# Optimization experiments

Measured on AMD Instinct MI355X. Metric: run time of the kernel, lower is better.

The kernel has to match this reference:

```python
import jax, jax.numpy as jnp
import numpy as np

V = 32000; D = 1024; H = 16; L = 2; T = 2048; B = 4; C = 32000
DH = D // H
EPS = 1e-5


def layernorm(x, g, b):
    mu = jnp.mean(x, axis=-1, keepdims=True)
    var = jnp.mean((x - mu) ** 2, axis=-1, keepdims=True)
    return (x - mu) * jax.lax.rsqrt(var + EPS) * g + b


def setup_inputs() -> dict:
    key = jax.random.key(0)
    ks = jax.random.split(key, 16)
    s = 0.02
    return {
        "tokens": jax.random.randint(ks[0], (B, T), 0, V),
        "embed_W": jax.random.normal(ks[1], (V, D), jnp.float32) * s,
        "pos_W": jax.random.normal(ks[2], (T, D), jnp.float32) * s,
        "ln_g": jnp.ones((L, D), jnp.float32),
        "ln_b": jnp.zeros((L, D), jnp.float32),
        "qkv_W": jax.random.normal(ks[3], (L, D, 3 * D), jnp.float32) * s,
        "qkv_b": jnp.zeros((L, 3 * D), jnp.float32),
        "out_W": jax.random.normal(ks[4], (L, D, D), jnp.float32) * s,
        "out_b": jnp.zeros((L, D), jnp.float32),
        "lnf_g": jnp.ones((D,), jnp.float32),
        "lnf_b": jnp.zeros((D,), jnp.float32),
        "head_W": jax.random.normal(ks[5], (D, C), jnp.float32) * s,
        "head_b": jnp.zeros((C,), jnp.float32),
    }


def attn_block(x, g, b, Wqkv, bqkv, Wo, bo):
    # pre-LN attention + residual. NOTE: original module defines an MLP but never calls it.
    h = layernorm(x, g, b)
    qkv = h @ Wqkv + bqkv                      # [B,T,3D]
    q, k, v = jnp.split(qkv, 3, axis=-1)
    q = q.reshape(B, T, H, DH)
    k = k.reshape(B, T, H, DH)
    v = v.reshape(B, T, H, DH)
    scores = jnp.einsum("bqhd,bkhd->bhqk", q, k) / np.sqrt(DH)
    causal = jnp.tril(jnp.ones((T, T), bool))
    scores = jnp.where(causal, scores, -jnp.inf)
    attn = jax.nn.softmax(scores, axis=-1)
    o = jnp.einsum("bhqk,bkhd->bqhd", attn, v).reshape(B, T, D)
    return x + o @ Wo + bo


def reference(tokens, embed_W, pos_W, ln_g, ln_b, qkv_W, qkv_b, out_W, out_b,
              lnf_g, lnf_b, head_W, head_b):
    h = embed_W[tokens] + pos_W[jnp.arange(T)][None, :, :]   # [B,T,D]
    for i in range(L):
        h = attn_block(h, ln_g[i], ln_b[i], qkv_W[i], qkv_b[i], out_W[i], out_b[i])
    h = layernorm(h, lnf_g, lnf_b)
    logits = h[:, -1] @ head_W + head_b                      # [B,C]
    return logits
```

## Files before the change

kernel.cpp:

```cpp
#include <hip/hip_runtime.h>

typedef __attribute__((ext_vector_type(8))) __bf16 bf16x8;
typedef __attribute__((ext_vector_type(4))) __bf16 bf16x4;
typedef __attribute__((ext_vector_type(4))) float f32x4;
typedef unsigned long long ull;

static constexpr int kB = 4, kT = 2048, kD = 1024, kH = 16;
static constexpr int kC = 32000, kM = 8192, k3D = 3072, kQK = 2048;

#define MFMA16(a, b, c) __builtin_amdgcn_mfma_f32_16x16x32_bf16((a), (b), (c), 0, 0, 0)

__device__ __forceinline__ void gload_lds16(const __bf16* g, __bf16* l) {
  __builtin_amdgcn_global_load_lds(
      (const __attribute__((address_space(1))) unsigned int*)(const void*)g,
      (__attribute__((address_space(3))) unsigned int*)(void*)l, 16, 0, 0);
}

__global__ __launch_bounds__(256) void prep_kernel(const float* __restrict__ qkv_W,
                                                   const float* __restrict__ out_W,
                                                   __bf16* __restrict__ WqkvT,
                                                   __bf16* __restrict__ WoT,
                                                   const int* __restrict__ tok,
                                                   const float* __restrict__ embW,
                                                   const float* __restrict__ posW,
                                                   const float* __restrict__ g,
                                                   const float* __restrict__ bb,
                                                   float* __restrict__ h,
                                                   __bf16* __restrict__ hn) {
  const int bid = blockIdx.x, tid = threadIdx.x;
  if (bid < 7168) {
    __shared__ float sh[32][33];
    const float* W; __bf16* WT; int N, tile;
    if (bid < 3072)      { W = qkv_W;                  WT = WqkvT;                  N = k3D; tile = bid; }
    else if (bid < 6144) { W = qkv_W + (size_t)kD*k3D; WT = WqkvT + (size_t)k3D*kD; N = k3D; tile = bid - 3072; }
    else                 { W = out_W;                  WT = WoT;                    N = kD;  tile = bid - 6144; }
    const int tx = tid & 31, ty = tid >> 5;
    const int ntile = N >> 5;
    const int c0 = (tile % ntile) << 5;
    const int r0 = (tile / ntile) << 5;
    #pragma unroll
    for (int i = 0; i < 4; i++) {
      const int r = ty + i * 8;
      sh[r][tx] = W[(size_t)(r0 + r) * N + c0 + tx];
    }
    __syncthreads();
    #pragma unroll
    for (int i = 0; i < 4; i++) {
      const int cc = ty + i * 8;
      WT[(size_t)(c0 + cc) * kD + r0 + tx] = (__bf16)sh[tx][cc];
    }
  } else {
    const int row = bid - 7168;
    const int t = row & (kT - 1);
    const int tk = tok[row];
    const f32x4 e = ((const f32x4*)(embW + (size_t)tk * kD))[tid];
    const f32x4 p = ((const f32x4*)(posW + (size_t)t * kD))[tid];
    const f32x4 xv = e + p;
    ((f32x4*)(h + (size_t)row * kD))[tid] = xv;
    float s  = xv[0] + xv[1] + xv[2] + xv[3];
    float s2 = xv[0]*xv[0] + xv[1]*xv[1] + xv[2]*xv[2] + xv[3]*xv[3];
    #pragma unroll
    for (int off = 1; off < 64; off <<= 1) {
      s  += __shfl_xor(s, off);
      s2 += __shfl_xor(s2, off);
    }
    __shared__ float red[8];
    const int w = tid >> 6;
    if ((tid & 63) == 0) { red[w*2] = s; red[w*2+1] = s2; }
    __syncthreads();
    s  = red[0] + red[2] + red[4] + red[6];
    s2 = red[1] + red[3] + red[5] + red[7];
    const float mu  = s * (1.f / kD);
    const float var = s2 * (1.f / kD) - mu * mu;
    const float rs  = rsqrtf(var + 1e-5f);
    const f32x4 gv = ((const f32x4*)g)[tid];
    const f32x4 bv = ((const f32x4*)bb)[tid];
    bf16x4 o;
    #pragma unroll
    for (int i = 0; i < 4; i++) o[i] = (__bf16)((xv[i] - mu) * rs * gv[i] + bv[i]);
    ((bf16x4*)(hn + (size_t)row * kD))[tid] = o;
  }
}

template <bool BF16OUT>
__global__ __launch_bounds__(256) void ln_kernel(const float* __restrict__ x,
                                                 const float* __restrict__ g,
                                                 const float* __restrict__ bb,
                                                 void* __restrict__ outp) {
  const int row = blockIdx.x, tid = threadIdx.x;
  const f32x4 xv = ((const f32x4*)(x + (size_t)row * kD))[tid];
  float s  = xv[0] + xv[1] + xv[2] + xv[3];
  float s2 = xv[0]*xv[0] + xv[1]*xv[1] + xv[2]*xv[2] + xv[3]*xv[3];
  #pragma unroll
  for (int off = 1; off < 64; off <<= 1) {
    s  += __shfl_xor(s, off);
    s2 += __shfl_xor(s2, off);
  }
  __shared__ float red[8];
  const int w = tid >> 6;
  if ((tid & 63) == 0) { red[w*2] = s; red[w*2+1] = s2; }
  __syncthreads();
  s  = red[0] + red[2] + red[4] + red[6];
  s2 = red[1] + red[3] + red[5] + red[7];
  const float mu  = s * (1.f / kD);
  const float var = s2 * (1.f / kD) - mu * mu;
  const float rs  = rsqrtf(var + 1e-5f);
  const f32x4 gv = ((const f32x4*)g)[tid];
  const f32x4 bv = ((const f32x4*)bb)[tid];
  if constexpr (BF16OUT) {
    bf16x4 o;
    #pragma unroll
    for (int i = 0; i < 4; i++) o[i] = (__bf16)((xv[i] - mu) * rs * gv[i] + bv[i]);
    ((bf16x4*)((__bf16*)outp + (size_t)row * kD))[tid] = o;
  } else {
    f32x4 o;
    #pragma unroll
    for (int i = 0; i < 4; i++) o[i] = (xv[i] - mu) * rs * gv[i] + bv[i];
    ((f32x4*)((float*)outp + (size_t)row * kD))[tid] = o;
  }
}

template <bool OUT_BF16>
__global__ __launch_bounds__(256) void gemm_bt_kernel(const __bf16* __restrict__ A,
                                                      const __bf16* __restrict__ BT,
                                                      const float* __restrict__ bias,
                                                      const float* resid,
                                                      float* outf,
                                                      __bf16* outb,
                                                      __bf16* vtp,
                                                      int N, int K, int ldc, int vt_c0,
                                                      int bm_mult, int bm_add) {
  __shared__ __bf16 As[128 * 64];
  __shared__ __bf16 Bs[128 * 64];
  const int tid = threadIdx.x;
  const int lane = tid & 63, w = tid >> 6;
  int wg = (int)blockIdx.x;
  const int nwg = gridDim.x;
  wg = (wg & 7) * (nwg >> 3) + (wg >> 3);
  const int nbn = N >> 7;
  const int bm = (wg / nbn) * bm_mult + bm_add;
  const int bn = wg % nbn;
  const int wr = (w >> 1) * 64, wc = (w & 1) * 64;
  const int lrow = lane & 15, lk8 = (lane >> 4) * 8;

  const int srow = lane >> 3;
  const int scol = (lane & 7) * 8;
  const __bf16* gA = A + (size_t)(bm * 128) * K;
  const __bf16* gB = BT + (size_t)(bn * 128) * K;

  f32x4 acc[4][4] = {};

  for (int k0 = 0; k0 < K; k0 += 64) {
    __syncthreads();
    #pragma unroll
    for (int i = 0; i < 4; i++) {
      const int c = w * 4 + i;
      const int row = c * 8 + srow;
      gload_lds16(gA + (size_t)row * K + k0 + scol, As + c * 512);
      gload_lds16(gB + (size_t)row * K + k0 + scol, Bs + c * 512);
    }
    __syncthreads();
    #pragma unroll
    for (int ks = 0; ks < 2; ks++) {
      bf16x8 af[4], bf[4];
      #pragma unroll
      for (int mt = 0; mt < 4; mt++)
        af[mt] = *(const bf16x8*)(As + (wr + mt * 16 + lrow) * 64 + ks * 32 + lk8);
      #pragma unroll
      for (int nt = 0; nt < 4; nt++)
        bf[nt] = *(const bf16x8*)(Bs + (wc + nt * 16 + lrow) * 64 + ks * 32 + lk8);
      __builtin_amdgcn_s_setprio(1);
      #pragma unroll
      for (int mt = 0; mt < 4; mt++)
        #pragma unroll
        for (int nt = 0; nt < 4; nt++)
          acc[mt][nt] = MFMA16(af[mt], bf[nt], acc[mt][nt]);
      __builtin_amdgcn_s_setprio(0);
    }
  }

  #pragma unroll
  for (int mt = 0; mt < 4; mt++) {
    const int row0 = bm * 128 + wr + mt * 16 + (lane >> 4) * 4;
    #pragma unroll
    for (int nt = 0; nt < 4; nt++) {
      const int col = bn * 128 + wc + nt * 16 + lrow;
      const float bsv = bias[col];
      if (vtp && col >= vt_c0) {
        const int vd = col - vt_c0;
        const int bb_ = row0 >> 11, t = row0 & (kT - 1);
        bf16x4 pk;
        #pragma unroll
        for (int r = 0; r < 4; r++) pk[r] = (__bf16)(acc[mt][nt][r] + bsv);
        *(bf16x4*)(vtp + ((size_t)((bb_ << 4) + (vd >> 6)) * 64 + (vd & 63)) * kT + t) = pk;
      } else {
        #pragma unroll
        for (int r = 0; r < 4; r++) {
          const size_t idx = (size_t)(row0 + r) * ldc + col;
          const float v = acc[mt][nt][r] + bsv;
          if constexpr (OUT_BF16) {
            outb[idx] = (__bf16)v;
          } else {
            outf[idx] = v + resid[idx];
          }
        }
      }
    }
  }
}

__global__ __launch_bounds__(256) void flash0_kernel(const __bf16* __restrict__ qkv,
                                                     const __bf16* __restrict__ vtg,
                                                     __bf16* __restrict__ o) {
  constexpr float SC = 0.18033688011112042f;
  __shared__ __bf16 Ks[64 * 64];
  __shared__ __bf16 Vs[64 * 64];
  const int tid = threadIdx.x, lane = tid & 63, w = tid >> 6;
  int wg = (int)blockIdx.x;
  const int nwg = gridDim.x;
  wg = (wg & 7) * (nwg >> 3) + (wg >> 3);
  const int sub = wg & 15, bh = wg >> 4;
  const int b = bh >> 4, hh = bh & 15;
  const int g = lane >> 4, qown = lane & 15;
  const int r8 = lane >> 3;
  const int sslot = (lane & 7) ^ (r8 & 7);
  const int swz = (qown & 7) << 3;
  const size_t row0 = (size_t)b * kT;

  for (int s = 0; s < 2; s++) {
    const int qt = s ? (31 - sub) : sub;

    const __bf16* qrow = qkv + (row0 + qt * 64 + w * 16 + qown) * kQK + hh * 64;
    bf16x8 qf[2];
    #pragma unroll
    for (int ks = 0; ks < 2; ks++) {
      bf16x8 qr = *(const bf16x8*)(qrow + ks * 32 + 8 * g);
      #pragma unroll
      for (int i = 0; i < 8; i++) qf[ks][i] = (__bf16)((float)qr[i] * SC);
    }

    float m_run = -1e30f, l_run = 0.f;
    f32x4 acc[4] = {};

    for (int kt = 0; kt <= qt; kt++) {
      __syncthreads();
      #pragma unroll
      for (int j = 0; j < 2; j++) {
        const int r = w * 16 + j * 8 + r8;
        gload_lds16(qkv + (row0 + kt * 64 + r) * kQK + 1024 + hh * 64 + sslot * 8,
                    Ks + (w * 16 + j * 8) * 64);
        gload_lds16(vtg + ((size_t)bh * 64 + r) * kT + kt * 64 + sslot * 8,
                    Vs + (w * 16 + j * 8) * 64);
      }
      __syncthreads();

      f32x4 sv[4] = {};
      #pragma unroll
      for (int nt = 0; nt < 4; nt++) {
        const int kr = nt * 16 + qown;
        #pragma unroll
        for (int ks = 0; ks < 2; ks++) {
          bf16x8 kf = *(const bf16x8*)(Ks + kr * 64 + ((ks * 32 + 8 * g) ^ swz));
          sv[nt] = MFMA16(kf, qf[ks], sv[nt]);
        }
      }
      if (kt == qt) {
        #pragma unroll
        for (int nt = 0; nt < 4; nt++)
          #pragma unroll
          for (int r = 0; r < 4; r++)
            if (nt * 16 + 4 * g + r > w * 16 + qown) sv[nt][r] = -1e30f;
      }

      float mx = -1e30f;
      #pragma unroll
      for (int nt = 0; nt < 4; nt++)
        #pragma unroll
        for (int r = 0; r < 4; r++) mx = fmaxf(mx, sv[nt][r]);
      mx = fmaxf(mx, __shfl_xor(mx, 16));
      mx = fmaxf(mx, __shfl_xor(mx, 32));

      float ps = 0.f;
      ull quad[4];
      if (__all(mx - m_run <= 8.0f)) {
        #pragma unroll
        for (int nt = 0; nt < 4; nt++) {
          union { bf16x4 v; ull u; } qd;
          #pragma unroll
          for (int r = 0; r < 4; r++) {
            const float p = exp2f(sv[nt][r] - m_run);
            ps += p;
            qd.v[r] = (__bf16)p;
          }
          quad[nt] = qd.u;
        }
        ps += __shfl_xor(ps, 16);
        ps += __shfl_xor(ps, 32);
        l_run += ps;
      } else {
        const float mnew = fmaxf(m_run, mx);
        const float fsc = exp2f(m_run - mnew);
        m_run = mnew;
        #pragma unroll
        for (int nt = 0; nt < 4; nt++) {
          union { bf16x4 v; ull u; } qd;
          #pragma unroll
          for (int r = 0; r < 4; r++) {
            const float p = exp2f(sv[nt][r] - mnew);
            ps += p;
            qd.v[r] = (__bf16)p;
          }
          quad[nt] = qd.u;
        }
        ps += __shfl_xor(ps, 16);
        ps += __shfl_xor(ps, 32);
        l_run = l_run * fsc + ps;
        float fr[4];
        #pragma unroll
        for (int r = 0; r < 4; r++) fr[r] = __shfl(fsc, 20 * g + r);
        #pragma unroll
        for (int nt = 0; nt < 4; nt++)
          #pragma unroll
          for (int r = 0; r < 4; r++) acc[nt][r] *= fr[r];
      }

      bf16x8 pf[2];
      #pragma unroll
      for (int ks = 0; ks < 2; ks++) {
        const int src = (g & 1) * 32 + qown;
        const ull t0 = __shfl(quad[2 * ks],     src);
        const ull t1 = __shfl(quad[2 * ks + 1], src);
        const ull lo = (g & 2) ? t1 : t0;
        const ull t2 = __shfl(quad[2 * ks],     src + 16);
        const ull t3 = __shfl(quad[2 * ks + 1], src + 16);
        const ull hi = (g & 2) ? t3 : t2;
        union { ull u[2]; bf16x8 v; } pk;
        pk.u[0] = lo; pk.u[1] = hi;
        pf[ks] = pk.v;
      }

      #pragma unroll
      for (int nt = 0; nt < 4; nt++) {
        const int vr = nt * 16 + qown;
        #pragma unroll
        for (int ks = 0; ks < 2; ks++) {
          bf16x8 vf = *(const bf16x8*)(Vs + vr * 64 + ((ks * 32 + 8 * g) ^ swz));
          acc[nt] = MFMA16(pf[ks], vf, acc[nt]);
        }
      }
    }

    const float li = 1.f / l_run;
    float lr[4];
    #pragma unroll
    for (int r = 0; r < 4; r++) lr[r] = __shfl(li, 20 * g + r);
    #pragma unroll
    for (int r = 0; r < 4; r++) {
      const int t = qt * 64 + w * 16 + 4 * g + r;
      #pragma unroll
      for (int nt = 0; nt < 4; nt++)
        o[(row0 + t) * kD + hh * 64 + nt * 16 + qown] = (__bf16)(acc[nt][r] * lr[r]);
    }
  }
}

__global__ __launch_bounds__(256) void flash1_kernel(const __bf16* __restrict__ qkv,
                                                     const __bf16* __restrict__ vtg,
                                                     float* __restrict__ part_acc,
                                                     float* __restrict__ part_ml) {
  constexpr float SC = 0.18033688011112042f;
  __shared__ __bf16 Ks[64 * 64];
  __shared__ __bf16 Vs[64 * 64];
  const int tid = threadIdx.x, lane = tid & 63, w = tid >> 6;
  int wg = (int)blockIdx.x;
  const int nwg = gridDim.x;
  wg = (wg & 7) * (nwg >> 3) + (wg >> 3);
  const int sub = wg & 7, bh = wg >> 3;
  const int b = bh >> 4, hh = bh & 15;
  const int g = lane >> 4, qown = lane & 15;
  const int r8 = lane >> 3;
  const int sslot = (lane & 7) ^ (r8 & 7);
  const int swz = (qown & 7) << 3;
  const size_t row0 = (size_t)b * kT;
  const int qt = 31, ktlo = sub * 4, kthi = ktlo + 4;

  const __bf16* qrow = qkv + (row0 + qt * 64 + w * 16 + qown) * kQK + hh * 64;
  bf16x8 qf[2];
  #pragma unroll
  for (int ks = 0; ks < 2; ks++) {
    bf16x8 qr = *(const bf16x8*)(qrow + ks * 32 + 8 * g);
    #pragma unroll
    for (int i = 0; i < 8; i++) qf[ks][i] = (__bf16)((float)qr[i] * SC);
  }

  float m_run = -1e30f, l_run = 0.f;
  f32x4 acc[4] = {};

  for (int kt = ktlo; kt < kthi; kt++) {
    __syncthreads();
    #pragma unroll
    for (int jj = 0; jj < 2; jj++) {
      const int r = w * 16 + jj * 8 + r8;
      gload_lds16(qkv + (row0 + kt * 64 + r) * kQK + 1024 + hh * 64 + sslot * 8,
                  Ks + (w * 16 + jj * 8) * 64);
      gload_lds16(vtg + ((size_t)bh * 64 + r) * kT + kt * 64 + sslot * 8,
                  Vs + (w * 16 + jj * 8) * 64);
    }
    __syncthreads();

    f32x4 sv[4] = {};
    #pragma unroll
    for (int nt = 0; nt < 4; nt++) {
      const int kr = nt * 16 + qown;
      #pragma unroll
      for (int ks = 0; ks < 2; ks++) {
        bf16x8 kf = *(const bf16x8*)(Ks + kr * 64 + ((ks * 32 + 8 * g) ^ swz));
        sv[nt] = MFMA16(kf, qf[ks], sv[nt]);
      }
    }
    if (kt == qt) {
      #pragma unroll
      for (int nt = 0; nt < 4; nt++)
        #pragma unroll
        for (int r = 0; r < 4; r++)
          if (nt * 16 + 4 * g + r > w * 16 + qown) sv[nt][r] = -1e30f;
    }

    float mx = -1e30f;
    #pragma unroll
    for (int nt = 0; nt < 4; nt++)
      #pragma unroll
      for (int r = 0; r < 4; r++) mx = fmaxf(mx, sv[nt][r]);
    mx = fmaxf(mx, __shfl_xor(mx, 16));
    mx = fmaxf(mx, __shfl_xor(mx, 32));

    const float mnew = fmaxf(m_run, mx);
    const float fsc = exp2f(m_run - mnew);
    m_run = mnew;
    float ps = 0.f;
    ull quad[4];
    #pragma unroll
    for (int nt = 0; nt < 4; nt++) {
      union { bf16x4 v; ull u; } qd;
      #pragma unroll
      for (int r = 0; r < 4; r++) {
        const float p = exp2f(sv[nt][r] - mnew);
        ps += p;
        qd.v[r] = (__bf16)p;
      }
      quad[nt] = qd.u;
    }
    ps += __shfl_xor(ps, 16);
    ps += __shfl_xor(ps, 32);
    l_run = l_run * fsc + ps;
    float fr[4];
    #pragma unroll
    for (int r = 0; r < 4; r++) fr[r] = __shfl(fsc, 20 * g + r);
    #pragma unroll
    for (int nt = 0; nt < 4; nt++)
      #pragma unroll
      for (int r = 0; r < 4; r++) acc[nt][r] *= fr[r];

    bf16x8 pf[2];
    #pragma unroll
    for (int ks = 0; ks < 2; ks++) {
      const int src = (g & 1) * 32 + qown;
      const ull t0 = __shfl(quad[2 * ks],     src);
      const ull t1 = __shfl(quad[2 * ks + 1], src);
      const ull lo = (g & 2) ? t1 : t0;
      const ull t2 = __shfl(quad[2 * ks],     src + 16);
      const ull t3 = __shfl(quad[2 * ks + 1], src + 16);
      const ull hi = (g & 2) ? t3 : t2;
      union { ull u[2]; bf16x8 v; } pk;
      pk.u[0] = lo; pk.u[1] = hi;
      pf[ks] = pk.v;
    }

    #pragma unroll
    for (int nt = 0; nt < 4; nt++) {
      const int vr = nt * 16 + qown;
      #pragma unroll
      for (int ks = 0; ks < 2; ks++) {
        bf16x8 vf = *(const bf16x8*)(Vs + vr * 64 + ((ks * 32 + 8 * g) ^ swz));
        acc[nt] = MFMA16(pf[ks], vf, acc[nt]);
      }
    }
  }

  const int tile = bh * 8 + sub;
  #pragma unroll
  for (int r = 0; r < 4; r++) {
    const int rr = w * 16 + 4 * g + r;
    #pragma unroll
    for (int nt = 0; nt < 4; nt++)
      part_acc[(size_t)tile * 4096 + rr * 64 + nt * 16 + qown] = acc[nt][r];
  }
  if (g == 0) {
    part_ml[tile * 128 + w * 16 + qown] = m_run;
    part_ml[tile * 128 + 64 + w * 16 + qown] = l_run;
  }
}

__global__ __launch_bounds__(256) void flash_merge_kernel(const float* __restrict__ part_acc,
                                                          const float* __restrict__ part_ml,
                                                          __bf16* __restrict__ o) {
  const int bh = blockIdx.x, b = bh >> 4, hh = bh & 15;
  for (int e = threadIdx.x; e < 4096; e += 256) {
    const int row = e >> 6, d = e & 63;
    float mstar = -1e30f;
    #pragma unroll
    for (int kc = 0; kc < 8; kc++)
      mstar = fmaxf(mstar, part_ml[(bh * 8 + kc) * 128 + row]);
    float lstar = 0.f, osum = 0.f;
    #pragma unroll
    for (int kc = 0; kc < 8; kc++) {
      const float wgt = exp2f(part_ml[(bh * 8 + kc) * 128 + row] - mstar);
      lstar += wgt * part_ml[(bh * 8 + kc) * 128 + 64 + row];
      osum  += wgt * part_acc[(size_t)(bh * 8 + kc) * 4096 + e];
    }
    o[(size_t)(b * kT + 1984 + row) * kD + hh * 64 + d] = (__bf16)(osum / lstar);
  }
}

__global__ __launch_bounds__(256) void proj_last_kernel(const __bf16* __restrict__ o,
                                                        const float* __restrict__ W,
                                                        const float* __restrict__ bias,
                                                        const float* __restrict__ h,
                                                        float* __restrict__ out4) {
  const int b = blockIdx.y;
  const int j = blockIdx.x * 256 + threadIdx.x;
  __shared__ float ov[kD];
  const __bf16* orow = o + (size_t)(b * kT + kT - 1) * kD;
  for (int i = threadIdx.x; i < kD; i += 256) ov[i] = (float)orow[i];
  __syncthreads();
  float acc = 0.f;
  #pragma unroll 8
  for (int k = 0; k < kD; k++) acc = fmaf(ov[k], W[(size_t)k * kD + j], acc);
  out4[b * kD + j] = h[(size_t)(b * kT + kT - 1) * kD + j] + bias[j] + acc;
}

__global__ __launch_bounds__(256) void head_kernel(const float* __restrict__ hl4,
                                                   const float* __restrict__ g,
                                                   const float* __restrict__ bb,
                                                   const float* __restrict__ W,
                                                   const float* __restrict__ hb,
                                                   float* __restrict__ out) {
  __shared__ float sh[kB * kD];
  __shared__ float red[4][kB][64];
  const int tid = threadIdx.x;
  const int wv = tid >> 6, ln = tid & 63;
  {
    const float* row = hl4 + wv * kD;
    float vals[16];
    float s = 0.f, s2 = 0.f;
    #pragma unroll
    for (int i = 0; i < 16; i++) {
      const float v = row[i * 64 + ln];
      vals[i] = v; s += v; s2 += v * v;
    }
    #pragma unroll
    for (int off = 1; off < 64; off <<= 1) {
      s += __shfl_xor(s, off); s2 += __shfl_xor(s2, off);
    }
    const float mu = s * (1.f / kD);
    const float rs = rsqrtf(s2 * (1.f / kD) - mu * mu + 1e-5f);
    #pragma unroll
    for (int i = 0; i < 16; i++) {
      const int c = i * 64 + ln;
      sh[wv * kD + c] = (vals[i] - mu) * rs * g[c] + bb[c];
    }
  }
  __syncthreads();
  const int jj = tid & 63, ks = tid >> 6;
  const int j = blockIdx.x * 64 + jj;
  float a[kB] = {};
  const int k0 = ks * 256;
  #pragma unroll 4
  for (int k = k0; k < k0 + 256; k++) {
    const float wvw = W[(size_t)k * kC + j];
    #pragma unroll
    for (int b2 = 0; b2 < kB; b2++) a[b2] = fmaf(sh[b2 * kD + k], wvw, a[b2]);
  }
  #pragma unroll
  for (int b2 = 0; b2 < kB; b2++) red[ks][b2][jj] = a[b2];
  __syncthreads();
  if (ks == 0) {
    const float bv = hb[j];
    #pragma unroll
    for (int b2 = 0; b2 < kB; b2++)
      out[(size_t)b2 * kC + j] = red[0][b2][jj] + red[1][b2][jj] + red[2][b2][jj] + red[3][b2][jj] + bv;
  }
}

extern "C" void kernel_launch(void* const* d_in, const int* in_sizes, int n_in,
                              void* d_out, int out_size, void* d_ws, size_t ws_size,
                              hipStream_t stream) {
  const int*   tokens = (const int*)d_in[0];
  const float* embW   = (const float*)d_in[1];
  const float* posW   = (const float*)d_in[2];
  const float* ln_g   = (const float*)d_in[3];
  const float* ln_b   = (const float*)d_in[4];
  const float* qkv_W  = (const float*)d_in[5];
  const float* qkv_b  = (const float*)d_in[6];
  const float* out_W  = (const float*)d_in[7];
  const float* out_b  = (const float*)d_in[8];
  const float* lnf_g  = (const float*)d_in[9];
  const float* lnf_b  = (const float*)d_in[10];
  const float* headW  = (const float*)d_in[11];
  const float* headb  = (const float*)d_in[12];
  float* logits = (float*)d_out;

  char* ws = (char*)d_ws;
  float*  h     = (float*)(ws);
  __bf16* hn    = (__bf16*)(ws + 33554432);
  __bf16* qkv   = (__bf16*)(ws + 50331648);
  __bf16* Vt    = (__bf16*)(ws + 83886080);
  __bf16* ob    = (__bf16*)(ws + 100663296);
  __bf16* WqkvT = (__bf16*)(ws + 117440512);
  __bf16* WoT   = (__bf16*)(ws + 130613248);
  float*  hl4   = (float*)(ws + 132710400);
  float* part_acc = (float*)(ws + 33554432);
  float* part_ml  = (float*)(ws + 33554432 + 8388608);

  prep_kernel<<<15360, 256, 0, stream>>>(qkv_W, out_W, WqkvT, WoT,
                                         tokens, embW, posW, ln_g, ln_b, h, hn);

  gemm_bt_kernel<true><<<(kM/128)*(k3D/128), 256, 0, stream>>>(
      hn, WqkvT, qkv_b, nullptr, nullptr, qkv, Vt, k3D, kD, kQK, 2048, 1, 0);
  flash0_kernel<<<kB*kH*16, 256, 0, stream>>>(qkv, Vt, ob);
  gemm_bt_kernel<false><<<(kM/128)*(kD/128), 256, 0, stream>>>(
      ob, WoT, out_b, h, h, nullptr, nullptr, kD, kD, kD, 1 << 30, 1, 0);

  ln_kernel<true><<<kM, 256, 0, stream>>>(h, ln_g + kD, ln_b + kD, hn);
  gemm_bt_kernel<true><<<(kM/128)*(2048/128), 256, 0, stream>>>(
      hn, WqkvT + (size_t)k3D*kD + (size_t)kD*kD, qkv_b + k3D + kD,
      nullptr, nullptr, qkv + 1024, Vt, 2048, kD, kQK, 1024, 1, 0);
  gemm_bt_kernel<true><<<kB*(kD/128), 256, 0, stream>>>(
      hn, WqkvT + (size_t)k3D*kD, qkv_b + k3D,
      nullptr, nullptr, qkv, nullptr, kD, kD, kQK, 1 << 30, 16, 15);
  flash1_kernel<<<kB*kH*8, 256, 0, stream>>>(qkv, Vt, part_acc, part_ml);
  flash_merge_kernel<<<kB*kH, 256, 0, stream>>>(part_acc, part_ml, ob);
  proj_last_kernel<<<dim3(kD/256, kB), 256, 0, stream>>>(ob, out_W + (size_t)kD*kD,
                                                         out_b + kD, h, hl4);
  head_kernel<<<kC/64, 256, 0, stream>>>(hl4, lnf_g, lnf_b, headW, headb, logits);
}
```

Before: 474.8 us.

## Share K/V tile loads across both paired query tiles in flash0

The flash0 kernel used to handle its two paired query tiles (sub and 31-sub) one after the other, reloading K/V tiles into LDS for each. Now a single pass over key tiles up to the larger query tile feeds both query tiles, and the smaller tile's update runs only while the key index is within its causal range. This roughly halves K/V global-to-LDS traffic and barrier count for the shorter tile. It doubles the live accumulator and Q-fragment registers, and the added launch-bounds occupancy hint of 4 blocks may force register spills.

Result: slower. 623.8 us (+31.4%).

```diff
diff --git a/kernel.cpp b/kernel.cpp
--- a/kernel.cpp
+++ b/kernel.cpp
@@ -209,9 +209,9 @@
   }
 }
 
-__global__ __launch_bounds__(256) void flash0_kernel(const __bf16* __restrict__ qkv,
-                                                     const __bf16* __restrict__ vtg,
-                                                     __bf16* __restrict__ o) {
+__global__ __launch_bounds__(256, 4) void flash0_kernel(const __bf16* __restrict__ qkv,
+                                                        const __bf16* __restrict__ vtg,
+                                                        __bf16* __restrict__ o) {
   constexpr float SC = 0.18033688011112042f;
   __shared__ __bf16 Ks[64 * 64];
   __shared__ __bf16 Vs[64 * 64];
@@ -226,34 +226,40 @@
   const int sslot = (lane & 7) ^ (r8 & 7);
   const int swz = (qown & 7) << 3;
   const size_t row0 = (size_t)b * kT;
-
-  for (int s = 0; s < 2; s++) {
-    const int qt = s ? (31 - sub) : sub;
-
-    const __bf16* qrow = qkv + (row0 + qt * 64 + w * 16 + qown) * kQK + hh * 64;
-    bf16x8 qf[2];
+  const int qt0 = sub, qt1 = 31 - sub;
+
+  bf16x8 qf0[2], qf1[2];
+  {
+    const __bf16* qr0p = qkv + (row0 + qt0 * 64 + w * 16 + qown) * kQK + hh * 64;
+    const __bf16* qr1p = qkv + (row0 + qt1 * 64 + w * 16 + qown) * kQK + hh * 64;
     #pragma unroll
     for (int ks = 0; ks < 2; ks++) {
-      bf16x8 qr = *(const bf16x8*)(qrow + ks * 32 + 8 * g);
-      #pragma unroll
-      for (int i = 0; i < 8; i++) qf[ks][i] = (__bf16)((float)qr[i] * SC);
-    }
-
-    float m_run = -1e30f, l_run = 0.f;
-    f32x4 acc[4] = {};
-
-    for (int kt = 0; kt <= qt; kt++) {
-      __syncthreads();
-      #pragma unroll
-      for (int j = 0; j < 2; j++) {
-        const int r = w * 16 + j * 8 + r8;
-        gload_lds16(qkv + (row0 + kt * 64 + r) * kQK + 1024 + hh * 64 + sslot * 8,
-                    Ks + (w * 16 + j * 8) * 64);
-        gload_lds16(vtg + ((size_t)bh * 64 + r) * kT + kt * 64 + sslot * 8,
-                    Vs + (w * 16 + j * 8) * 64);
-      }
-      __syncthreads();
-
+      bf16x8 qa = *(const bf16x8*)(qr0p + ks * 32 + 8 * g);
+      bf16x8 qb = *(const bf16x8*)(qr1p + ks * 32 + 8 * g);
+      #pragma unroll
+      for (int i = 0; i < 8; i++) {
+        qf0[ks][i] = (__bf16)((float)qa[i] * SC);
+        qf1[ks][i] = (__bf16)((float)qb[i] * SC);
+      }
+    }
+  }
+
+  float m0 = -1e30f, l0 = 0.f, m1 = -1e30f, l1 = 0.f;
+  f32x4 acc0[4] = {}, acc1[4] = {};
+
+  for (int kt = 0; kt <= qt1; kt++) {
+    __syncthreads();
+    #pragma unroll
+    for (int j = 0; j < 2; j++) {
+      const int r = w * 16 + j * 8 + r8;
+      gload_lds16(qkv + (row0 + kt * 64 + r) * kQK + 1024 + hh * 64 + sslot * 8,
+                  Ks + (w * 16 + j * 8) * 64);
+      gload_lds16(vtg + ((size_t)bh * 64 + r) * kT + kt * 64 + sslot * 8,
+                  Vs + (w * 16 + j * 8) * 64);
+    }
+    __syncthreads();
+
+    {
       f32x4 sv[4] = {};
       #pragma unroll
       for (int nt = 0; nt < 4; nt++) {
@@ -261,10 +267,10 @@
         #pragma unroll
         for (int ks = 0; ks < 2; ks++) {
           bf16x8 kf = *(const bf16x8*)(Ks + kr * 64 + ((ks * 32 + 8 * g) ^ swz));
-          sv[nt] = MFMA16(kf, qf[ks], sv[nt]);
-        }
-      }
-      if (kt == qt) {
+          sv[nt] = MFMA16(kf, qf1[ks], sv[nt]);
+        }
+      }
+      if (kt == qt1) {
         #pragma unroll
         for (int nt = 0; nt < 4; nt++)
           #pragma unroll
@@ -282,13 +288,13 @@
 
       float ps = 0.f;
       ull quad[4];
-      if (__all(mx - m_run <= 8.0f)) {
+      if (__all(mx - m1 <= 8.0f)) {
         #pragma unroll
         for (int nt = 0; nt < 4; nt++) {
           union { bf16x4 v; ull u; } qd;
           #pragma unroll
           for (int r = 0; r < 4; r++) {
-            const float p = exp2f(sv[nt][r] - m_run);
+            const float p = exp2f(sv[nt][r] - m1);
             ps += p;
             qd.v[r] = (__bf16)p;
           }
@@ -296,11 +302,11 @@
         }
         ps += __shfl_xor(ps, 16);
         ps += __shfl_xor(ps, 32);
-        l_run += ps;
+        l1 += ps;
       } else {
-        const float mnew = fmaxf(m_run, mx);
-        const float fsc = exp2f(m_run - mnew);
-        m_run = mnew;
+        const float mnew = fmaxf(m1, mx);
+        const float fsc = exp2f(m1 - mnew);
+        m1 = mnew;
         #pragma unroll
         for (int nt = 0; nt < 4; nt++) {
           union { bf16x4 v; ull u; } qd;
@@ -314,14 +320,14 @@
         }
         ps += __shfl_xor(ps, 16);
         ps += __shfl_xor(ps, 32);
-        l_run = l_run * fsc + ps;
+        l1 = l1 * fsc + ps;
         float fr[4];
         #pragma unroll
         for (int r = 0; r < 4; r++) fr[r] = __shfl(fsc, 20 * g + r);
         #pragma unroll
         for (int nt = 0; nt < 4; nt++)
           #pragma unroll
-          for (int r = 0; r < 4; r++) acc[nt][r] *= fr[r];
+          for (int r = 0; r < 4; r++) acc1[nt][r] *= fr[r];
       }
 
       bf16x8 pf[2];
@@ -345,21 +351,133 @@
         #pragma unroll
         for (int ks = 0; ks < 2; ks++) {
           bf16x8 vf = *(const bf16x8*)(Vs + vr * 64 + ((ks * 32 + 8 * g) ^ swz));
-          acc[nt] = MFMA16(pf[ks], vf, acc[nt]);
-        }
-      }
-    }
-
-    const float li = 1.f / l_run;
+          acc1[nt] = MFMA16(pf[ks], vf, acc1[nt]);
+        }
+      }
+    }
+
+    if (kt <= qt0) {
+      f32x4 sv[4] = {};
+      #pragma unroll
+      for (int nt = 0; nt < 4; nt++) {
+        const int kr = nt * 16 + qown;
+        #pragma unroll
+        for (int ks = 0; ks < 2; ks++) {
+          bf16x8 kf = *(const bf16x8*)(Ks + kr * 64 + ((ks * 32 + 8 * g) ^ swz));
+          sv[nt] = MFMA16(kf, qf0[ks], sv[nt]);
+        }
+      }
+      if (kt == qt0) {
+        #pragma unroll
+        for (int nt = 0; nt < 4; nt++)
+          #pragma unroll
+          for (int r = 0; r < 4; r++)
+            if (nt * 16 + 4 * g + r > w * 16 + qown) sv[nt][r] = -1e30f;
+      }
+
+      float mx = -1e30f;
+      #pragma unroll
+      for (int nt = 0; nt < 4; nt++)
+        #pragma unroll
+        for (int r = 0; r < 4; r++) mx = fmaxf(mx, sv[nt][r]);
+      mx = fmaxf(mx, __shfl_xor(mx, 16));
+      mx = fmaxf(mx, __shfl_xor(mx, 32));
+
+      float ps = 0.f;
+      ull quad[4];
+      if (__all(mx - m0 <= 8.0f)) {
+        #pragma unroll
+        for (int nt = 0; nt < 4; nt++) {
+          union { bf16x4 v; ull u; } qd;
+          #pragma unroll
+          for (int r = 0; r < 4; r++) {
+            const float p = exp2f(sv[nt][r] - m0);
+            ps += p;
+            qd.v[r] = (__bf16)p;
+          }
+          quad[nt] = qd.u;
+        }
+        ps += __shfl_xor(ps, 16);
+        ps += __shfl_xor(ps, 32);
+        l0 += ps;
+      } else {
+        const float mnew = fmaxf(m0, mx);
+        const float fsc = exp2f(m0 - mnew);
+        m0 = mnew;
+        #pragma unroll
+        for (int nt = 0; nt < 4; nt++) {
+          union { bf16x4 v; ull u; } qd;
+          #pragma unroll
+          for (int r = 0; r < 4; r++) {
+            const float p = exp2f(sv[nt][r] - mnew);
+            ps += p;
+            qd.v[r] = (__bf16)p;
+          }
+          quad[nt] = qd.u;
+        }
+        ps += __shfl_xor(ps, 16);
+        ps += __shfl_xor(ps, 32);
+        l0 = l0 * fsc + ps;
+        float fr[4];
+        #pragma unroll
+        for (int r = 0; r < 4; r++) fr[r] = __shfl(fsc, 20 * g + r);
+        #pragma unroll
+        for (int nt = 0; nt < 4; nt++)
+          #pragma unroll
+          for (int r = 0; r < 4; r++) acc0[nt][r] *= fr[r];
+      }
+
+      bf16x8 pf[2];
+      #pragma unroll
+      for (int ks = 0; ks < 2; ks++) {
+        const int src = (g & 1) * 32 + qown;
+        const ull t0 = __shfl(quad[2 * ks],     src);
+        const ull t1 = __shfl(quad[2 * ks + 1], src);
+        const ull lo = (g & 2) ? t1 : t0;
+        const ull t2 = __shfl(quad[2 * ks],     src + 16);
+        const ull t3 = __shfl(quad[2 * ks + 1], src + 16);
+        const ull hi = (g & 2) ? t3 : t2;
+        union { ull u[2]; bf16x8 v; } pk;
+        pk.u[0] = lo; pk.u[1] = hi;
+        pf[ks] = pk.v;
+      }
+
+      #pragma unroll
+      for (int nt = 0; nt < 4; nt++) {
+        const int vr = nt * 16 + qown;
+        #pragma unroll
+        for (int ks = 0; ks < 2; ks++) {
+          bf16x8 vf = *(const bf16x8*)(Vs + vr * 64 + ((ks * 32 + 8 * g) ^ swz));
+          acc0[nt] = MFMA16(pf[ks], vf, acc0[nt]);
+        }
+      }
+    }
+  }
+
+  {
+    const float li = 1.f / l1;
     float lr[4];
     #pragma unroll
     for (int r = 0; r < 4; r++) lr[r] = __shfl(li, 20 * g + r);
     #pragma unroll
     for (int r = 0; r < 4; r++) {
-      const int t = qt * 64 + w * 16 + 4 * g + r;
+      const int t = qt1 * 64 + w * 16 + 4 * g + r;
       #pragma unroll
       for (int nt = 0; nt < 4; nt++)
-        o[(row0 + t) * kD + hh * 64 + nt * 16 + qown] = (__bf16)(acc[nt][r] * lr[r]);
+        o[(row0 + t) * kD + hh * 64 + nt * 16 + qown] = (__bf16)(acc1[nt][r] * lr[r]);
+    }
+  }
+  {
+    const float li = 1.f / l0;
+    float lr[4];
+    #pragma unroll
+    for (int r = 0; r < 4; r++) lr[r] = __shfl(li, 20 * g + r);
+    #pragma unroll
+    for (int r = 0; r < 4; r++) {
+      const int t = qt0 * 64 + w * 16 + 4 * g + r;
+      #pragma unroll
+      for (int nt = 0; nt < 4; nt++)
+        o[(row0 + t) * kD + hh * 64 + nt * 16 + qown] = (__bf16)(acc0[nt][r] * lr[r]);
     }
   }
 }
```
